# Optimization experiments

Measured on AMD Instinct MI355X. Metric: run time of the kernel, lower is better.

Reference implementation:

```python
import jax, jax.numpy as jnp
import numpy as np

B_IN, C, K, P, STRIDE, ITERS = 32, 32, 3, 4, 2, 3
PSIZE = P * P


def _patch(t):
    # t: (b, h, w, B, d) -> (b, oh, ow, K, K, B, d), matching torch fancy-index patching
    b, h, w = t.shape[:3]
    oh = int((h - K + 1) / STRIDE)
    idx = (np.arange(oh) * STRIDE)[:, None] + np.arange(K)[None, :]  # (oh, K)
    t = t[:, idx]          # (b, oh, K, w, B, d)
    t = t[:, :, :, idx]    # (b, oh, K, ow, K, B, d)
    perm = (0, 1, 3, 2, 4) + tuple(range(5, t.ndim))
    return jnp.transpose(t, perm), oh, oh


def _forward(x, a, weights, beta_u, beta_a):
    b = x.shape[0]
    KKB = K * K * B_IN
    p_in, oh, ow = _patch(x)
    a_in, _, _ = _patch(a)
    pose = p_in.reshape(b, oh, ow, KKB, P, P)
    a_in = a_in.reshape(b, oh, ow, KKB, 1)
    # voting: per-capsule 4x4 matmul with transformation matrices
    v = jnp.einsum('bhwnij,ncjl->bhwncil', pose, weights).reshape(b, oh, ow, KKB, C, PSIZE)
    eps = 1e-6
    lam = 1e-3
    ln2pi = np.float32(np.log(2.0 * np.pi))
    mu = sigma_sq = a_out = None
    for it in range(ITERS):
        if it == 0:
            r = jnp.full((b, oh, ow, KKB, C), 1.0 / C, jnp.float32) * a_in  # a_in broadcasts over C
        else:
            # gaussian log-likelihood of each vote under each output capsule
            ln_pjh = -(v - mu) ** 2 / (2.0 * sigma_sq) - 0.5 * jnp.log(sigma_sq) - 0.5 * ln2pi
            ln_ap = ln_pjh.sum(axis=5) + jnp.log(a_out.reshape(b, oh, ow, 1, C))
            r = jax.nn.softmax(ln_ap, axis=4)
        r_sum = r.sum(axis=3, keepdims=True)               # (b,oh,ow,1,C)
        coeff = (r / (r_sum + eps))[..., None]             # (b,oh,ow,KKB,C,1)
        mu = (coeff * v).sum(axis=3, keepdims=True)        # (b,oh,ow,1,C,PSIZE)
        sigma_sq = (coeff * (v - mu) ** 2).sum(axis=3, keepdims=True) + eps
        # beta_u: (C,1) broadcasts against (...,C,PSIZE); log(sqrt(s)) == 0.5*log(s)
        cost_h = (beta_u + 0.5 * jnp.log(sigma_sq)) * r_sum[..., None]
        a_out = jax.nn.sigmoid(lam * (beta_a - cost_h.sum(axis=5, keepdims=True)))
    p_out = mu.reshape(b, oh, ow, C, PSIZE)
    a_out = a_out.reshape(b, oh, ow, C, 1)
    return p_out, a_out


def setup_inputs() -> dict:
    key = jax.random.key(0)
    k1, k2, k3, k4, k5 = jax.random.split(key, 5)
    x = jax.random.normal(k1, (8, 14, 14, B_IN, PSIZE), jnp.float32)
    a = jax.random.uniform(k2, (8, 14, 14, B_IN, 1), jnp.float32)
    weights = jax.random.normal(k3, (K * K * B_IN, C, P, P), jnp.float32)
    beta_u = jax.random.normal(k4, (C, 1), jnp.float32) * 0.1
    beta_a = jax.random.normal(k5, (C, 1), jnp.float32) * 0.1
    return {"x": x, "a": a, "weights": weights, "beta_u": beta_u, "beta_a": beta_a}


def reference(x, a, weights, beta_u, beta_a):
    return _forward(x, a, weights, beta_u, beta_a)
```

## Files before the change

kernel.cpp:

```cpp
#include <hip/hip_runtime.h>

#define TPB 512

__global__ __launch_bounds__(TPB) void convcaps_kernel(
    const float* __restrict__ xg,
    const float* __restrict__ ag,
    const float* __restrict__ wg,
    const float* __restrict__ bu,
    const float* __restrict__ ba,
    float* __restrict__ outp)
{
    __shared__ __align__(16) float pose_s[4608];
    __shared__ float a_s[288];
    __shared__ __align__(16) float scratch[8448];
    __shared__ float rsum_part[256];
    __shared__ float mu_tab[512];
    __shared__ float i2s_tab[512];
    __shared__ float aout_tab[32];
    __shared__ float Kc_tab[32];

    const int tid = threadIdx.x;
    const int pos = blockIdx.x;
    const int bb  = pos / 36;
    const int rem = pos % 36;
    const int yy  = rem / 6;
    const int xx  = rem % 6;

    #pragma unroll
    for (int wi = 0; wi < 9; ++wi) {
        const int kh = wi / 3, kw = wi % 3;
        const float* src =
            xg + (size_t)((((bb * 14) + (2 * yy + kh)) * 14 + (2 * xx + kw)) * 32) * 16;
        pose_s[wi * 512 + tid] = src[tid];
    }
    if (tid < 288) {
        const int wi = tid >> 5, bi = tid & 31;
        const int kh = wi / 3, kw = wi % 3;
        a_s[tid] = ag[(size_t)(((bb * 14) + (2 * yy + kh)) * 14 + (2 * xx + kw)) * 32 + bi];
    }
    __syncthreads();

    const int c    = tid & 31;
    const int s    = tid >> 5;
    const int lane = tid & 63;
    const int wv   = tid >> 6;
    const float4* wp = (const float4*)wg;

    for (int it = 0; it < 3; ++it) {
        float mu_c[16], i2s_c[16], Kc = 0.f;
        if (it > 0) {
            #pragma unroll
            for (int p = 0; p < 16; ++p) {
                mu_c[p]  = mu_tab[c * 16 + p];
                i2s_c[p] = i2s_tab[c * 16 + p];
            }
            Kc = Kc_tab[c];
        }
        float macc[16], vacc[16], rs = 0.f;
        #pragma unroll
        for (int p = 0; p < 16; ++p) { macc[p] = 0.f; vacc[p] = 0.f; }

        for (int k = 0; k < 18; ++k) {
            const int n = s * 18 + k;
            const float4* pp = (const float4*)&pose_s[n << 4];
            float pf[16];
            float4 q;
            q = pp[0]; pf[0]=q.x; pf[1]=q.y; pf[2]=q.z;  pf[3]=q.w;
            q = pp[1]; pf[4]=q.x; pf[5]=q.y; pf[6]=q.z;  pf[7]=q.w;
            q = pp[2]; pf[8]=q.x; pf[9]=q.y; pf[10]=q.z; pf[11]=q.w;
            q = pp[3]; pf[12]=q.x; pf[13]=q.y; pf[14]=q.z; pf[15]=q.w;
            const int wbase = (n * 32 + c) * 4;
            float wf[16];
            float4 w0 = wp[wbase + 0]; wf[0]=w0.x;  wf[1]=w0.y;  wf[2]=w0.z;  wf[3]=w0.w;
            float4 w1 = wp[wbase + 1]; wf[4]=w1.x;  wf[5]=w1.y;  wf[6]=w1.z;  wf[7]=w1.w;
            float4 w2 = wp[wbase + 2]; wf[8]=w2.x;  wf[9]=w2.y;  wf[10]=w2.z; wf[11]=w2.w;
            float4 w3 = wp[wbase + 3]; wf[12]=w3.x; wf[13]=w3.y; wf[14]=w3.z; wf[15]=w3.w;
            float v[16];
            #pragma unroll
            for (int i = 0; i < 4; ++i)
                #pragma unroll
                for (int l = 0; l < 4; ++l)
                    v[i*4+l] = pf[i*4+0] * wf[0*4+l] + pf[i*4+1] * wf[1*4+l]
                             + pf[i*4+2] * wf[2*4+l] + pf[i*4+3] * wf[3*4+l];
            float r;
            if (it == 0) {
                r = a_s[n] * 0.03125f;
            } else {
                float t = 0.f;
                #pragma unroll
                for (int p = 0; p < 16; ++p) {
                    float d = v[p] - mu_c[p];
                    t = fmaf(d * d, i2s_c[p], t);
                }
                float lnap = -t - Kc;
                float m = lnap;
                #pragma unroll
                for (int msk = 16; msk >= 1; msk >>= 1) m = fmaxf(m, __shfl_xor(m, msk));
                float e = __expf(lnap - m);
                float sum = e;
                #pragma unroll
                for (int msk = 16; msk >= 1; msk >>= 1) sum += __shfl_xor(sum, msk);
                r = e / sum;
            }
            rs += r;
            #pragma unroll
            for (int p = 0; p < 16; ++p) {
                float rv = r * v[p];
                macc[p] += rv;
                vacc[p] = fmaf(rv, v[p], vacc[p]);
            }
        }

        #pragma unroll
        for (int p = 0; p < 16; ++p) {
            macc[p] += __shfl_xor(macc[p], 32);
            vacc[p] += __shfl_xor(vacc[p], 32);
        }
        rs += __shfl_xor(rs, 32);
        if (lane < 32) {
            const int base = (wv * 32 + lane) * 33;
            #pragma unroll
            for (int p = 0; p < 16; ++p) {
                scratch[base + p]      = macc[p];
                scratch[base + 16 + p] = vacc[p];
            }
            rsum_part[wv * 32 + lane] = rs;
        }
        __syncthreads();

        const int fc = tid >> 4, fp = tid & 15;
        float ms = 0.f, vs = 0.f, rsc = 0.f;
        #pragma unroll
        for (int w = 0; w < 8; ++w) {
            ms  += scratch[(w * 32 + fc) * 33 + fp];
            vs  += scratch[(w * 32 + fc) * 33 + 16 + fp];
            rsc += rsum_part[w * 32 + fc];
        }
        const float inv = 1.f / (rsc + 1e-6f);
        const float S   = rsc * inv;
        const float mu  = ms * inv;
        const float sig = vs * inv - mu * mu * (2.f - S) + 1e-6f;
        const float lg  = __logf(sig);
        float lgs = lg;
        #pragma unroll
        for (int msk = 8; msk >= 1; msk >>= 1) lgs += __shfl_xor(lgs, msk);
        const float buv  = bu[fc];
        const float bav  = ba[fc];
        const float cost = rsc * (16.f * buv + 0.5f * lgs);
        const float ao   = 1.f / (1.f + __expf(-0.001f * (bav - cost)));

        mu_tab[fc * 16 + fp]  = mu;
        i2s_tab[fc * 16 + fp] = 0.5f / sig;
        if (fp == 0) {
            aout_tab[fc] = ao;
            Kc_tab[fc]   = 0.5f * lgs - __logf(ao);
        }

        if (it == 2) {
            outp[(size_t)pos * 512 + tid] = mu;
            if (fp == 0) outp[147456 + (size_t)pos * 32 + fc] = ao;
        }
        __syncthreads();
    }
}

extern "C" void kernel_launch(void* const* d_in, const int* in_sizes, int n_in,
                              void* d_out, int out_size, void* d_ws, size_t ws_size,
                              hipStream_t stream) {
    (void)in_sizes; (void)n_in; (void)out_size; (void)d_ws; (void)ws_size;
    const float* x  = (const float*)d_in[0];
    const float* a  = (const float*)d_in[1];
    const float* w  = (const float*)d_in[2];
    const float* bu = (const float*)d_in[3];
    const float* ba = (const float*)d_in[4];
    float* out = (float*)d_out;
    convcaps_kernel<<<dim3(288), dim3(TPB), 0, stream>>>(x, a, w, bu, ba, out);
}
```

Measured before the change: 148.6 us.

## Split routing over input-capsule chunks across blocks with per-iteration kernels

The single kernel ran only 288 blocks, one per output position, on a GPU with many CUs. The new path splits the 288 input capsules of each position into 3 chunks of 96, each handled by its own block, and writes partial sums of mu, variance and r to workspace. One kernel runs per EM iteration, each rebuilding mu and sigma from the previous partials, and a final kernel produces the outputs. This raises the block count to 864 for better CU occupancy, at the cost of four launches, global round-trips and recomputing votes on every pass. The old kernel stays as a fallback when the workspace is too small.

```diff
diff --git a/kernel.cpp b/kernel.cpp
--- a/kernel.cpp
+++ b/kernel.cpp
@@ -1,6 +1,214 @@
 #include <hip/hip_runtime.h>
 
 #define TPB 512
+#define APB 512
+#define NPOS 288
+#define NCH 3
+#define CHUNK 96
+#define PSTRIDE 1056
+
+
+template<int IT>
+__global__ __launch_bounds__(APB, 4) void caps_acc(
+    const float* __restrict__ xg,
+    const float* __restrict__ ag,
+    const float* __restrict__ wg,
+    const float* __restrict__ bu,
+    const float* __restrict__ ba,
+    const float* __restrict__ pin,
+    float* __restrict__ pout)
+{
+    __shared__ __align__(16) float pose_s[CHUNK * 16];
+    __shared__ float a_s[CHUNK];
+    __shared__ __align__(16) float scratch[8 * 32 * 33];
+    __shared__ float rsum_part[8 * 32];
+    __shared__ float mu_tab[512];
+    __shared__ float i2s_tab[512];
+    __shared__ float Kc_tab[32];
+
+    const int tid = threadIdx.x;
+    const int blk = blockIdx.x;
+    const int pos = blk / NCH;
+    const int ch  = blk - pos * NCH;
+    const int bb  = pos / 36;
+    const int rem = pos % 36;
+    const int yy  = rem / 6;
+    const int xx  = rem % 6;
+
+    #pragma unroll
+    for (int j = 0; j < 3; ++j) {
+        const float* src =
+            xg + (size_t)((((bb * 14) + (2 * yy + ch)) * 14 + (2 * xx + j)) * 32) * 16;
+        pose_s[j * 512 + tid] = src[tid];
+    }
+    if (IT == 0) {
+        if (tid < CHUNK) {
+            const int j = tid >> 5, bi = tid & 31;
+            a_s[tid] = ag[(size_t)(((bb * 14) + (2 * yy + ch)) * 14 + (2 * xx + j)) * 32 + bi];
+        }
+    }
+
+    const int fc = tid >> 4, fp = tid & 15;
+    if (IT > 0) {
+        const float* q0 = pin + (size_t)pos * (NCH * PSTRIDE) + fc * 33;
+        float ms = 0.f, vs = 0.f, rsc = 0.f;
+        #pragma unroll
+        for (int cc = 0; cc < NCH; ++cc) {
+            const float* q = q0 + cc * PSTRIDE;
+            ms  += q[fp];
+            vs  += q[16 + fp];
+            rsc += q[32];
+        }
+        const float inv = 1.f / (rsc + 1e-6f);
+        const float S   = rsc * inv;
+        const float mu  = ms * inv;
+        const float sig = vs * inv - mu * mu * (2.f - S) + 1e-6f;
+        const float lg  = __logf(sig);
+        float lgs = lg;
+        #pragma unroll
+        for (int msk = 8; msk >= 1; msk >>= 1) lgs += __shfl_xor(lgs, msk);
+        const float cost = rsc * (16.f * bu[fc] + 0.5f * lgs);
+        const float ao   = 1.f / (1.f + __expf(-0.001f * (ba[fc] - cost)));
+        mu_tab[tid]  = mu;
+        i2s_tab[tid] = 0.5f / sig;
+        if (fp == 0) Kc_tab[fc] = 0.5f * lgs - __logf(ao);
+    }
+    __syncthreads();
+
+    const int c    = tid & 31;
+    const int s    = tid >> 5;
+    const int lane = tid & 63;
+    const int wv   = tid >> 6;
+    const float4* wp = (const float4*)wg;
+
+    float mu_c[16], i2s_c[16], Kc = 0.f;
+    if (IT > 0) {
+        #pragma unroll
+        for (int p = 0; p < 16; ++p) {
+            mu_c[p]  = mu_tab[c * 16 + p];
+            i2s_c[p] = i2s_tab[c * 16 + p];
+        }
+        Kc = Kc_tab[c];
+    }
+    float macc[16], vacc[16], rs = 0.f;
+    #pragma unroll
+    for (int p = 0; p < 16; ++p) { macc[p] = 0.f; vacc[p] = 0.f; }
+
+    for (int k = 0; k < 6; ++k) {
+        const int nl = s * 6 + k;
+        const int n  = ch * CHUNK + nl;
+        const float4* pp = (const float4*)&pose_s[nl << 4];
+        float pf[16];
+        float4 q;
+        q = pp[0]; pf[0]=q.x;  pf[1]=q.y;  pf[2]=q.z;  pf[3]=q.w;
+        q = pp[1]; pf[4]=q.x;  pf[5]=q.y;  pf[6]=q.z;  pf[7]=q.w;
+        q = pp[2]; pf[8]=q.x;  pf[9]=q.y;  pf[10]=q.z; pf[11]=q.w;
+        q = pp[3]; pf[12]=q.x; pf[13]=q.y; pf[14]=q.z; pf[15]=q.w;
+        const int wbase = (n * 32 + c) * 4;
+        float wf[16];
+        float4 w0 = wp[wbase + 0]; wf[0]=w0.x;  wf[1]=w0.y;  wf[2]=w0.z;  wf[3]=w0.w;
+        float4 w1 = wp[wbase + 1]; wf[4]=w1.x;  wf[5]=w1.y;  wf[6]=w1.z;  wf[7]=w1.w;
+        float4 w2 = wp[wbase + 2]; wf[8]=w2.x;  wf[9]=w2.y;  wf[10]=w2.z; wf[11]=w2.w;
+        float4 w3 = wp[wbase + 3]; wf[12]=w3.x; wf[13]=w3.y; wf[14]=w3.z; wf[15]=w3.w;
+        float v[16];
+        #pragma unroll
+        for (int i = 0; i < 4; ++i)
+            #pragma unroll
+            for (int l = 0; l < 4; ++l)
+                v[i*4+l] = pf[i*4+0] * wf[0*4+l] + pf[i*4+1] * wf[1*4+l]
+                         + pf[i*4+2] * wf[2*4+l] + pf[i*4+3] * wf[3*4+l];
+        float r;
+        if (IT == 0) {
+            r = a_s[nl] * 0.03125f;
+        } else {
+            float t0 = 0.f, t1 = 0.f, t2 = 0.f, t3 = 0.f;
+            #pragma unroll
+            for (int p = 0; p < 16; p += 4) {
+                float d0 = v[p]   - mu_c[p];   t0 = fmaf(d0*d0, i2s_c[p],   t0);
+                float d1 = v[p+1] - mu_c[p+1]; t1 = fmaf(d1*d1, i2s_c[p+1], t1);
+                float d2 = v[p+2] - mu_c[p+2]; t2 = fmaf(d2*d2, i2s_c[p+2], t2);
+                float d3 = v[p+3] - mu_c[p+3]; t3 = fmaf(d3*d3, i2s_c[p+3], t3);
+            }
+            float lnap = -((t0 + t1) + (t2 + t3)) - Kc;
+            float m = lnap;
+            #pragma unroll
+            for (int msk = 16; msk >= 1; msk >>= 1) m = fmaxf(m, __shfl_xor(m, msk));
+            float e = __expf(lnap - m);
+            float sum = e;
+            #pragma unroll
+            for (int msk = 16; msk >= 1; msk >>= 1) sum += __shfl_xor(sum, msk);
+            r = e / sum;
+        }
+        rs += r;
+        #pragma unroll
+        for (int p = 0; p < 16; ++p) {
+            float rv = r * v[p];
+            macc[p] += rv;
+            vacc[p] = fmaf(rv, v[p], vacc[p]);
+        }
+    }
+
+    #pragma unroll
+    for (int p = 0; p < 16; ++p) {
+        macc[p] += __shfl_xor(macc[p], 32);
+        vacc[p] += __shfl_xor(vacc[p], 32);
+    }
+    rs += __shfl_xor(rs, 32);
+    if (lane < 32) {
+        const int base = (wv * 32 + lane) * 33;
+        #pragma unroll
+        for (int p = 0; p < 16; ++p) {
+            scratch[base + p]      = macc[p];
+            scratch[base + 16 + p] = vacc[p];
+        }
+        rsum_part[wv * 32 + lane] = rs;
+    }
+    __syncthreads();
+
+    float ms = 0.f, vs = 0.f, rsc = 0.f;
+    #pragma unroll
+    for (int w = 0; w < 8; ++w) {
+        ms  += scratch[(w * 32 + fc) * 33 + fp];
+        vs  += scratch[(w * 32 + fc) * 33 + 16 + fp];
+        rsc += rsum_part[w * 32 + fc];
+    }
+    float* po = pout + (size_t)(pos * NCH + ch) * PSTRIDE + fc * 33;
+    po[fp]      = ms;
+    po[16 + fp] = vs;
+    if (fp == 0) po[32] = rsc;
+}
+
+__global__ __launch_bounds__(512) void caps_fin(
+    const float* __restrict__ pin,
+    const float* __restrict__ bu,
+    const float* __restrict__ ba,
+    float* __restrict__ outp)
+{
+    const int tid = threadIdx.x;
+    const int pos = blockIdx.x;
+    const int fc = tid >> 4, fp = tid & 15;
+    const float* q0 = pin + (size_t)pos * (NCH * PSTRIDE) + fc * 33;
+    float ms = 0.f, vs = 0.f, rsc = 0.f;
+    #pragma unroll
+    for (int cc = 0; cc < NCH; ++cc) {
+        const float* q = q0 + cc * PSTRIDE;
+        ms  += q[fp];
+        vs  += q[16 + fp];
+        rsc += q[32];
+    }
+    const float inv = 1.f / (rsc + 1e-6f);
+    const float S   = rsc * inv;
+    const float mu  = ms * inv;
+    const float sig = vs * inv - mu * mu * (2.f - S) + 1e-6f;
+    const float lg  = __logf(sig);
+    float lgs = lg;
+    #pragma unroll
+    for (int msk = 8; msk >= 1; msk >>= 1) lgs += __shfl_xor(lgs, msk);
+    const float cost = rsc * (16.f * bu[fc] + 0.5f * lgs);
+    const float ao   = 1.f / (1.f + __expf(-0.001f * (ba[fc] - cost)));
+    outp[(size_t)pos * 512 + tid] = mu;
+    if (fp == 0) outp[147456 + (size_t)pos * 32 + fc] = ao;
+}
 
 __global__ __launch_bounds__(TPB) void convcaps_kernel(
     const float* __restrict__ xg,
@@ -167,12 +375,24 @@
 extern "C" void kernel_launch(void* const* d_in, const int* in_sizes, int n_in,
                               void* d_out, int out_size, void* d_ws, size_t ws_size,
                               hipStream_t stream) {
-    (void)in_sizes; (void)n_in; (void)out_size; (void)d_ws; (void)ws_size;
+    (void)in_sizes; (void)n_in; (void)out_size;
     const float* x  = (const float*)d_in[0];
     const float* a  = (const float*)d_in[1];
     const float* w  = (const float*)d_in[2];
     const float* bu = (const float*)d_in[3];
     const float* ba = (const float*)d_in[4];
     float* out = (float*)d_out;
-    convcaps_kernel<<<dim3(288), dim3(TPB), 0, stream>>>(x, a, w, bu, ba, out);
+
+    const size_t buf_elems = (size_t)NPOS * NCH * PSTRIDE;
+    if (ws_size < 2 * buf_elems * sizeof(float)) {
+        convcaps_kernel<<<dim3(288), dim3(TPB), 0, stream>>>(x, a, w, bu, ba, out);
+        return;
+    }
+    float* buf0 = (float*)d_ws;
+    float* buf1 = buf0 + buf_elems;
+
+    caps_acc<0><<<dim3(NPOS * NCH), dim3(APB), 0, stream>>>(x, a, w, bu, ba, nullptr, buf0);
+    caps_acc<1><<<dim3(NPOS * NCH), dim3(APB), 0, stream>>>(x, a, w, bu, ba, buf0, buf1);
+    caps_acc<2><<<dim3(NPOS * NCH), dim3(APB), 0, stream>>>(x, a, w, bu, ba, buf1, buf0);
+    caps_fin<<<dim3(NPOS), dim3(512), 0, stream>>>(buf0, bu, ba, out);
 }
```

Result: slower. 209.8 us (+41.2%).
